# Kernel tuning notes

Measured on AMD Instinct MI355X. Metric: run time of the kernel, lower is better.

## Reference

```python
import jax, jax.numpy as jnp
import numpy as np

HEADS = 8

def _ln(x, g, b):
    m = jnp.mean(x, -1, keepdims=True)
    v = jnp.mean((x - m) ** 2, -1, keepdims=True)
    return (x - m) * jax.lax.rsqrt(v + 1e-5) * g + b

def _l2n(t):
    n = jnp.sqrt(jnp.sum(t * t, -1, keepdims=True))
    return t / jnp.maximum(n, 1e-12)

def _xca(x, ln_g, ln_b, w_qkv, temp, w_out, b_out):
    B, H, W, D = x.shape
    n = H * W
    xf = x.reshape(B, n, D)
    h = _ln(xf, ln_g, ln_b)
    qkv = h @ w_qkv  # [B, n, 3*inner]
    q, k, v = jnp.split(qkv, 3, axis=-1)
    def tohd(t):
        return t.reshape(B, n, HEADS, -1).transpose(0, 2, 3, 1)  # b h d n
    q, k, v = tohd(q), tohd(k), tohd(v)
    q, k = _l2n(q), _l2n(k)
    sim = jnp.einsum('bhdn,bhen->bhde', q, k) * jnp.exp(temp)[None, :, None, None]
    attn = jax.nn.softmax(sim, axis=-1)
    out = jnp.einsum('bhde,bhen->bhdn', attn, v)
    out = out.transpose(0, 3, 1, 2).reshape(B, n, -1)  # b n (h d)
    return (out @ w_out + b_out).reshape(B, H, W, D)

def _dwconv(x, w, b):
    # x: [B,C,H,W], w: [C,1,k,k] depthwise
    y = jax.lax.conv_general_dilated(x, w, (1, 1), 'SAME',
                                     feature_group_count=x.shape[1],
                                     dimension_numbers=('NCHW', 'OIHW', 'NCHW'))
    return y + b[None, :, None, None]

def _lpi(x, ln_g, ln_b, w1, b1, bn_g, bn_b, w2, b2):
    h = _ln(x, ln_g, ln_b).transpose(0, 3, 1, 2)  # b c h w
    h = _dwconv(h, w1, b1)
    # BatchNorm2d (training-mode batch stats, biased var, eps=1e-5)
    m = jnp.mean(h, (0, 2, 3), keepdims=True)
    v = jnp.mean((h - m) ** 2, (0, 2, 3), keepdims=True)
    h = (h - m) * jax.lax.rsqrt(v + 1e-5) * bn_g[None, :, None, None] + bn_b[None, :, None, None]
    h = jax.nn.gelu(h, approximate=False)
    h = _dwconv(h, w2, b2)
    return h.transpose(0, 2, 3, 1)

def _ff(x, g, b, w1, b1, w2, b2):
    h = _ln(x, g, b)
    h = jax.nn.gelu(h @ w1 + b1, approximate=False)
    return h @ w2 + b2

def setup_inputs() -> dict:
    key = jax.random.key(0)
    D, depth, Hh, dh, M = 384, 4, 8, 48, 1536
    inner = Hh * dh
    B, H, W = 16, 48, 48
    ks = jax.random.split(key, 8)
    x = jax.random.normal(ks[0], (B, H, W, D), jnp.float32)
    def nrm(k, shape, s=0.02):
        return jax.random.normal(k, shape, jnp.float32) * s
    return dict(
        x=x,
        ln1_g=jnp.ones((depth, D)), ln1_b=jnp.zeros((depth, D)),
        w_qkv=nrm(ks[1], (depth, D, 3 * inner)),
        temp=jnp.ones((depth, Hh)),
        w_out=nrm(ks[2], (depth, inner, D)), b_out=jnp.zeros((depth, D)),
        scale_attn=jnp.full((depth, D), 0.1, jnp.float32),
        lpi_ln_g=jnp.ones((depth, D)), lpi_ln_b=jnp.zeros((depth, D)),
        conv1_w=nrm(ks[3], (depth, D, 1, 3, 3), 0.1), conv1_b=jnp.zeros((depth, D)),
        bn_g=jnp.ones((depth, D)), bn_b=jnp.zeros((depth, D)),
        conv2_w=nrm(ks[4], (depth, D, 1, 3, 3), 0.1), conv2_b=jnp.zeros((depth, D)),
        scale_lpi=jnp.full((depth, D), 0.1, jnp.float32),
        ff_ln_g=jnp.ones((depth, D)), ff_ln_b=jnp.zeros((depth, D)),
        w1=nrm(ks[5], (depth, D, M)), b1=jnp.zeros((depth, M)),
        w2=nrm(ks[6], (depth, M, D)), b2=jnp.zeros((depth, D)),
        scale_ff=jnp.full((depth, D), 0.1, jnp.float32),
    )

def reference(x, ln1_g, ln1_b, w_qkv, temp, w_out, b_out, scale_attn,
              lpi_ln_g, lpi_ln_b, conv1_w, conv1_b, bn_g, bn_b, conv2_w, conv2_b, scale_lpi,
              ff_ln_g, ff_ln_b, w1, b1, w2, b2, scale_ff):
    depth = ln1_g.shape[0]
    for i in range(depth):
        x = _xca(x, ln1_g[i], ln1_b[i], w_qkv[i], temp[i], w_out[i], b_out[i]) * scale_attn[i] + x
        x = _lpi(x, lpi_ln_g[i], lpi_ln_b[i], conv1_w[i], conv1_b[i], bn_g[i], bn_b[i], conv2_w[i], conv2_b[i]) * scale_lpi[i] + x
        x = _ff(x, ff_ln_g[i], ff_ln_b[i], w1[i], b1[i], w2[i], b2[i]) * scale_ff[i] + x
    return x
```

## Files before the change

### kernel.cpp

```cpp
#include <hip/hip_runtime.h>
#include <math.h>

typedef unsigned short u16;
typedef unsigned int   u32;
typedef u16   u16x8 __attribute__((ext_vector_type(8)));
typedef u16   u16x4 __attribute__((ext_vector_type(4)));
typedef short s16x8 __attribute__((ext_vector_type(8)));
typedef float f32x4 __attribute__((ext_vector_type(4)));

#define DEVFN static __device__ __forceinline__
#define GLOBAL_AS __attribute__((address_space(1)))
#define LDS_AS    __attribute__((address_space(3)))

constexpr int Bb = 16, Hh = 48, Ww = 48, Dd = 384;
constexpr int Nn = Hh * Ww;
constexpr int NT = Bb * Nn;
constexpr int NH = 8, DHd = 48;
constexpr int INNER = NH * DHd;
constexpr int QC = 3 * INNER;
constexpr int MF = 1536;
constexpr int DEPTH = 4;
constexpr int NCH = 6;

DEVFN float bf2f(u16 u) { return __uint_as_float(((u32)u) << 16); }
DEVFN u16   f2bu(float f) { u32 x = __float_as_uint(f); return (u16)((x + 0x7FFFu + ((x >> 16) & 1u)) >> 16); }
DEVFN float geluf(float x) { return 0.5f * x * (1.0f + erff(x * 0.70710678118654752440f)); }

DEVFN void gload16(const u16* g, u16* lds_base) {
    __builtin_amdgcn_global_load_lds((const GLOBAL_AS void*)g, (LDS_AS void*)lds_base, 16, 0, 0);
}

__global__ void k_copy(const float* __restrict__ in, float* __restrict__ X) {
    size_t i0 = ((size_t)blockIdx.x * 256 + threadIdx.x) * 4;
    *(f32x4*)(X + i0) = *(const f32x4*)(in + i0);
}

__global__ __launch_bounds__(256) void k_trb(const float* __restrict__ in, u16* __restrict__ out,
                                             int K, int N) {
    __shared__ float tile[64][65];
    in  += (size_t)blockIdx.z * K * N;
    out += (size_t)blockIdx.z * K * N;
    int k0 = blockIdx.y * 64, n0 = blockIdx.x * 64;
    int t = threadIdx.x;
    int r = t >> 4, c = (t & 15) * 4;
#pragma unroll
    for (int j = 0; j < 4; j++) {
        f32x4 v = *(const f32x4*)&in[(size_t)(k0 + r + j * 16) * N + n0 + c];
        tile[r + j * 16][c] = v[0]; tile[r + j * 16][c + 1] = v[1];
        tile[r + j * 16][c + 2] = v[2]; tile[r + j * 16][c + 3] = v[3];
    }
    __syncthreads();
#pragma unroll
    for (int j = 0; j < 4; j++) {
        u16x4 o;
#pragma unroll
        for (int i = 0; i < 4; i++) o[i] = f2bu(tile[c + i][r + j * 16]);
        *(u16x4*)&out[(size_t)(n0 + r + j * 16) * K + k0 + c] = o;
    }
}

__global__ __launch_bounds__(256) void k_ln(const float* __restrict__ X,
                                            const float* __restrict__ g, const float* __restrict__ bta,
                                            u16* __restrict__ out) {
    int row = blockIdx.x * 4 + (threadIdx.x >> 6);
    int lane = threadIdx.x & 63;
    const float* xr = X + (size_t)row * Dd;
    float v[6]; float s = 0.f, s2 = 0.f;
#pragma unroll
    for (int j = 0; j < 6; j++) { v[j] = xr[lane + 64 * j]; s += v[j]; s2 += v[j] * v[j]; }
#pragma unroll
    for (int off = 32; off >= 1; off >>= 1) { s += __shfl_down(s, off); s2 += __shfl_down(s2, off); }
    s = __shfl(s, 0); s2 = __shfl(s2, 0);
    float m = s * (1.0f / Dd);
    float rstd = 1.0f / sqrtf(s2 * (1.0f / Dd) - m * m + 1e-5f);
    u16* orow = out + (size_t)row * Dd;
#pragma unroll
    for (int j = 0; j < 6; j++) {
        int c = lane + 64 * j;
        orow[c] = f2bu((v[j] - m) * rstd * g[c] + bta[c]);
    }
}

__global__ __launch_bounds__(256) void k_lnstat(const float* __restrict__ X, float* __restrict__ LNS) {
    int row = blockIdx.x * 4 + (threadIdx.x >> 6);
    int lane = threadIdx.x & 63;
    const float* xr = X + (size_t)row * Dd;
    float s = 0.f, s2 = 0.f;
#pragma unroll
    for (int j = 0; j < 6; j++) { float v = xr[lane + 64 * j]; s += v; s2 += v * v; }
#pragma unroll
    for (int off = 32; off >= 1; off >>= 1) { s += __shfl_down(s, off); s2 += __shfl_down(s2, off); }
    if (lane == 0) {
        float m = s * (1.0f / Dd);
        float rstd = 1.0f / sqrtf(s2 * (1.0f / Dd) - m * m + 1e-5f);
        LNS[row * 2] = m;
        LNS[row * 2 + 1] = rstd;
    }
}

template <int MODE>
__global__ __launch_bounds__(512, 4) void k_mgemm(const u16* __restrict__ A, const u16* __restrict__ BT,
                                                  int Kdim, int Ndim,
                                                  const float* __restrict__ bias, const float* __restrict__ scale,
                                                  float* __restrict__ Xres, u16* __restrict__ Out) {
    __shared__ __align__(16) u16 Ts[3][24 * 512];
    const int gridX = Ndim >> 7;
    const int nwg = gridX * (NT >> 8);
    const int cpx = nwg >> 3;
    const int id = blockIdx.x;
    const int id2 = (id & 7) * cpx + (id >> 3);
    const int n0 = (id2 % gridX) * 128;
    const int m0 = (id2 / gridX) * 256;
    const int t = threadIdx.x;
    const int w = t >> 6, l = t & 63;
    const int wm = w >> 1, wn = w & 1;
    const int lr = l >> 2;
    const int sc = ((l & 3) ^ (lr & 3)) * 8;
    const int fr = l & 15, rq = l >> 4;
    const int c0 = w * 3;

    auto stage = [&](int buf, int k0) {
#pragma unroll
        for (int j = 0; j < 3; j++) {
            const int c = c0 + j;
            const u16* src = (c < 16)
                ? A  + (size_t)(m0 + c * 16 + lr) * Kdim + k0 + sc
                : BT + (size_t)(n0 + (c - 16) * 16 + lr) * Kdim + k0 + sc;
            gload16(src, Ts[buf] + c * 512);
        }
    };

    const int nt = Kdim >> 5;
    stage(0, 0);
    stage(1, 32);

    f32x4 acc[4][4] = {};
    for (int kt = 0; kt < nt; ++kt) {
        if (kt + 1 < nt) {
            asm volatile("s_waitcnt vmcnt(3)" ::: "memory");
        } else {
            asm volatile("s_waitcnt vmcnt(0)" ::: "memory");
        }
        __builtin_amdgcn_s_barrier();
        __builtin_amdgcn_sched_barrier(0);
        if (kt + 2 < nt) stage((kt + 2) % 3, (kt + 2) * 32);
        const u16* ts = Ts[kt % 3];
        s16x8 af[4], bf[4];
#pragma unroll
        for (int f = 0; f < 4; f++) {
            const int row = wm * 64 + f * 16 + fr;
            af[f] = *(const s16x8*)&ts[row * 32 + ((rq ^ (fr & 3)) * 8)];
        }
#pragma unroll
        for (int g = 0; g < 4; g++) {
            const int row = wn * 64 + g * 16 + fr;
            bf[g] = *(const s16x8*)&ts[8192 + row * 32 + ((rq ^ (fr & 3)) * 8)];
        }
#pragma unroll
        for (int f = 0; f < 4; f++)
#pragma unroll
            for (int g = 0; g < 4; g++)
                acc[f][g] = __builtin_amdgcn_mfma_f32_16x16x32_bf16(af[f], bf[g], acc[f][g], 0, 0, 0);
    }
#pragma unroll
    for (int g = 0; g < 4; g++) {
        const int n = n0 + wn * 64 + g * 16 + fr;
        float bv = (MODE != 0) ? bias[n] : 0.f;
        float sv = (MODE == 2) ? scale[n] : 0.f;
#pragma unroll
        for (int f = 0; f < 4; f++) {
            const size_t i0 = (size_t)(m0 + wm * 64 + f * 16 + rq * 4);
#pragma unroll
            for (int r = 0; r < 4; r++) {
                float v = acc[f][g][r];
                if (MODE == 0) {
                    Out[(i0 + r) * Ndim + n] = f2bu(v);
                } else if (MODE == 1) {
                    Out[(i0 + r) * Ndim + n] = f2bu(geluf(v + bv));
                } else {
                    float* xr = Xres + (i0 + r) * Ndim + n;
                    *xr += sv * (v + bv);
                }
            }
        }
    }
}

__global__ __launch_bounds__(256) void k_nrm_part(const u16* __restrict__ QKV, float* __restrict__ part) {
    int b = blockIdx.x, s = blockIdx.y;
    int t = threadIdx.x;
    float a0 = 0, a1 = 0, a2 = 0;
    for (int r = s * 96; r < (s + 1) * 96; r++) {
        const u16* row = QKV + (size_t)(b * Nn + r) * QC;
        float v0 = bf2f(row[t]), v1 = bf2f(row[t + 256]), v2 = bf2f(row[t + 512]);
        a0 += v0 * v0; a1 += v1 * v1; a2 += v2 * v2;
    }
    float* o = part + (size_t)(b * 24 + s) * 768;
    o[t] = a0; o[t + 256] = a1; o[t + 512] = a2;
}

__global__ void k_nrm_fin(const float* __restrict__ part, float* __restrict__ INVN) {
    int idx = blockIdx.x * 256 + threadIdx.x;
    int b = idx / 768, c = idx - b * 768;
    float s = 0;
#pragma unroll
    for (int k = 0; k < 24; k++) s += part[(size_t)(b * 24 + k) * 768 + c];
    INVN[idx] = 1.0f / fmaxf(sqrtf(s), 1e-12f);
}

__global__ __launch_bounds__(256) void k_sim(const u16* __restrict__ QKV, float* __restrict__ SIMP) {
    const int bh = blockIdx.x;
    const int b = bh >> 3, h = bh & 7;
    const int chunk = blockIdx.y;
    __shared__ float qt[48][65];
    __shared__ float kt[48][65];
    const int t = threadIdx.x;
    const int w = t >> 6, l = t & 63;
    const int fr = l & 15, rq = l >> 4;
    const int ti0 = w, ti1 = w + 4;
    f32x4 acc0 = {}, acc1 = {}, acc2 = {};

    auto doTile = [&](int ti, f32x4& a) {
        const int d0 = (ti / 3) * 16, e0 = (ti % 3) * 16;
#pragma unroll
        for (int s = 0; s < 2; s++) {
            const float* qp = &qt[d0 + fr][s * 32 + rq * 8];
            const float* kp = &kt[e0 + fr][s * 32 + rq * 8];
            s16x8 af, bf;
#pragma unroll
            for (int j = 0; j < 8; j++) {
                af[j] = (short)(__float_as_uint(qp[j]) >> 16);
                bf[j] = (short)(__float_as_uint(kp[j]) >> 16);
            }
            a = __builtin_amdgcn_mfma_f32_16x16x32_bf16(af, bf, a, 0, 0, 0);
        }
    };

    for (int c0 = chunk * (Nn / NCH); c0 < (chunk + 1) * (Nn / NCH); c0 += 64) {
        __syncthreads();
        for (int e = t; e < 48 * 64; e += 256) {
            int r = e / 48, d = e - r * 48;
            const u16* p = QKV + (size_t)(b * Nn + c0 + r) * QC + h * DHd + d;
            qt[d][r] = bf2f(p[0]);
            kt[d][r] = bf2f(p[INNER]);
        }
        __syncthreads();
        doTile(ti0, acc0);
        doTile(ti1, acc1);
        if (w == 0) doTile(8, acc2);
    }

    float* so = SIMP + ((size_t)chunk * (Bb * NH) + bh) * (DHd * DHd);
    auto wr = [&](int ti, const f32x4& a) {
        const int d0 = (ti / 3) * 16, e0 = (ti % 3) * 16;
#pragma unroll
        for (int r = 0; r < 4; r++) so[(d0 + rq * 4 + r) * DHd + e0 + fr] = a[r];
    };
    wr(ti0, acc0);
    wr(ti1, acc1);
    if (w == 0) wr(8, acc2);
}

__global__ __launch_bounds__(256) void k_smax(const float* __restrict__ SIMP, float* __restrict__ SIM,
                                              const float* __restrict__ INVN, const float* __restrict__ temp) {
    int wid = blockIdx.x * 4 + (threadIdx.x >> 6);
    int lane = threadIdx.x & 63;
    int b = wid / (NH * DHd); int rem = wid - b * NH * DHd; int h = rem / DHd; int d = rem - h * DHd;
    int bh = b * NH + h;
    float et = expf(temp[h]);
    float invq = INVN[b * 768 + h * DHd + d];
    float myv = 0.f, mv = -3.0e38f;
    if (lane < DHd) {
        float s = 0.f;
#pragma unroll
        for (int c = 0; c < NCH; c++)
            s += SIMP[((size_t)c * (Bb * NH) + bh) * (DHd * DHd) + d * DHd + lane];
        myv = s * invq * INVN[b * 768 + 384 + h * DHd + lane] * et;
        mv = myv;
    }
#pragma unroll
    for (int off = 32; off >= 1; off >>= 1) mv = fmaxf(mv, __shfl_down(mv, off));
    mv = __shfl(mv, 0);
    float e = (lane < DHd) ? expf(myv - mv) : 0.f;
    float s = e;
#pragma unroll
    for (int off = 32; off >= 1; off >>= 1) s += __shfl_down(s, off);
    s = __shfl(s, 0);
    if (lane < DHd) SIM[(size_t)bh * (DHd * DHd) + d * DHd + lane] = e / s;
}

__global__ __launch_bounds__(256) void k_av(const u16* __restrict__ QKV, const float* __restrict__ SIM,
                                            u16* __restrict__ AOUT) {
    const int bh = blockIdx.x;
    const int b = bh >> 3, h = bh & 7;
    __shared__ __align__(16) float at[48][52];
    const int t = threadIdx.x;
    for (int e = t; e < 48 * 48; e += 256) at[e / 48][e % 48] = SIM[(size_t)bh * (DHd * DHd) + e];
    __syncthreads();
    const int r = blockIdx.y * 256 + t;
    const u16x8* vp = (const u16x8*)(QKV + (size_t)(b * Nn + r) * QC + 2 * INNER + h * DHd);
    f32x4 vv[12];
#pragma unroll
    for (int q8 = 0; q8 < 6; q8++) {
        u16x8 u = vp[q8];
#pragma unroll
        for (int j = 0; j < 8; j++) vv[q8 * 2 + (j >> 2)][j & 3] = bf2f(u[j]);
    }
    u16x8 ob[6];
#pragma unroll
    for (int d = 0; d < 48; d++) {
        f32x4 sv = {0.f, 0.f, 0.f, 0.f};
#pragma unroll
        for (int e4 = 0; e4 < 12; e4++) sv += *(const f32x4*)&at[d][e4 * 4] * vv[e4];
        ob[d >> 3][d & 7] = f2bu(sv[0] + sv[1] + sv[2] + sv[3]);
    }
    u16x8* orow = (u16x8*)(AOUT + (size_t)(b * Nn + r) * Dd + h * DHd);
#pragma unroll
    for (int q8 = 0; q8 < 6; q8++) orow[q8] = ob[q8];
}

__global__ __launch_bounds__(384) void k_lpi1(const float* __restrict__ X, const float* __restrict__ LNS,
                                              const float* __restrict__ g, const float* __restrict__ bta,
                                              const float* __restrict__ wgt, const float* __restrict__ cbias,
                                              u16* __restrict__ CF, float* __restrict__ BNP) {
    const int c = threadIdx.x;
    const int by = blockIdx.x;
    const int y = by % Hh, b = by / Hh;
    const int x0 = blockIdx.y * (Ww / 2);
    float w9[9];
#pragma unroll
    for (int j = 0; j < 9; j++) w9[j] = wgt[c * 9 + j];
    const float gc = g[c], bc = bta[c], cb = cbias[c];
    const size_t base = (size_t)b * Nn * Dd;
    const float* lns = LNS + (size_t)b * Nn * 2;

    auto load3 = [&](int xx, float* col) {
        if (xx < 0 || xx >= Ww) { col[0] = col[1] = col[2] = 0.f; return; }
#pragma unroll
        for (int dy = 0; dy < 3; dy++) {
            int yy = y + dy - 1;
            if (yy < 0 || yy >= Hh) { col[dy] = 0.f; }
            else {
                int tok = yy * Ww + xx;
                float m = lns[tok * 2], r = lns[tok * 2 + 1];
                col[dy] = (X[base + (size_t)tok * Dd + c] - m) * r * gc + bc;
            }
        }
    };

    float A[3], B[3], C[3], T[3];
    load3(x0 - 1, A); load3(x0, B); load3(x0 + 1, C);
    float s = 0.f, s2 = 0.f;
    u16* crow = CF + base + ((size_t)y * Ww + x0) * Dd + c;
    for (int x = x0; x < x0 + Ww / 2; x++) {
        load3(x + 2, T);
        float acc = cb;
#pragma unroll
        for (int dy = 0; dy < 3; dy++)
            acc += w9[dy * 3] * A[dy] + w9[dy * 3 + 1] * B[dy] + w9[dy * 3 + 2] * C[dy];
        crow[(size_t)(x - x0) * Dd] = f2bu(acc);
        s += acc; s2 += acc * acc;
#pragma unroll
        for (int dy = 0; dy < 3; dy++) { A[dy] = B[dy]; B[dy] = C[dy]; C[dy] = T[dy]; }
    }
    float* o = BNP + ((size_t)by * 2 + blockIdx.y) * 768;
    o[c] = s; o[384 + c] = s2;
}

__global__ __launch_bounds__(384) void k_bnred1(const float* __restrict__ BNP, float* __restrict__ BNQ) {
    int t = threadIdx.x, blk = blockIdx.x;
    float s = 0.f, s2 = 0.f;
    for (int i = blk * 24; i < blk * 24 + 24; i++) { s += BNP[(size_t)i * 768 + t]; s2 += BNP[(size_t)i * 768 + 384 + t]; }
    BNQ[(size_t)blk * 768 + t] = s; BNQ[(size_t)blk * 768 + 384 + t] = s2;
}

__global__ __launch_bounds__(384) void k_bnred2(const float* __restrict__ BNQ,
                                                const float* __restrict__ bng, const float* __restrict__ bnb,
                                                float* __restrict__ BNC) {
    int t = threadIdx.x;
    float s = 0.f, s2 = 0.f;
    for (int i = 0; i < 64; i++) { s += BNQ[(size_t)i * 768 + t]; s2 += BNQ[(size_t)i * 768 + 384 + t]; }
    float m = s / NT;
    float var = s2 / NT - m * m;
    float r = 1.0f / sqrtf(var + 1e-5f);
    BNC[t] = r * bng[t];
    BNC[384 + t] = bnb[t] - m * r * bng[t];
}

__global__ __launch_bounds__(384) void k_lpi2(const u16* __restrict__ CF, const float* __restrict__ BNC,
                                              const float* __restrict__ wgt, const float* __restrict__ cbias,
                                              const float* __restrict__ scale, float* __restrict__ X) {
    const int c = threadIdx.x;
    const int by = blockIdx.x;
    const int y = by % Hh, b = by / Hh;
    const int x0 = blockIdx.y * (Ww / 2);
    float w9[9];
#pragma unroll
    for (int j = 0; j < 9; j++) w9[j] = wgt[c * 9 + j];
    const float bnA = BNC[c], bnB = BNC[384 + c];
    const float cb = cbias[c], sc = scale[c];
    const size_t base = (size_t)b * Nn * Dd;

    auto load3 = [&](int xx, float* col) {
        if (xx < 0 || xx >= Ww) { col[0] = col[1] = col[2] = 0.f; return; }
#pragma unroll
        for (int dy = 0; dy < 3; dy++) {
            int yy = y + dy - 1;
            if (yy < 0 || yy >= Hh) { col[dy] = 0.f; }
            else {
                int tok = yy * Ww + xx;
                col[dy] = geluf(bf2f(CF[base + (size_t)tok * Dd + c]) * bnA + bnB);
            }
        }
    };

    float A[3], B[3], C[3], T[3];
    load3(x0 - 1, A); load3(x0, B); load3(x0 + 1, C);
    float* xrow = X + base + ((size_t)y * Ww + x0) * Dd + c;
    for (int x = x0; x < x0 + Ww / 2; x++) {
        load3(x + 2, T);
        float acc = cb;
#pragma unroll
        for (int dy = 0; dy < 3; dy++)
            acc += w9[dy * 3] * A[dy] + w9[dy * 3 + 1] * B[dy] + w9[dy * 3 + 2] * C[dy];
        xrow[(size_t)(x - x0) * Dd] += sc * acc;
#pragma unroll
        for (int dy = 0; dy < 3; dy++) { A[dy] = B[dy]; B[dy] = C[dy]; C[dy] = T[dy]; }
    }
}

extern "C" void kernel_launch(void* const* d_in, const int* in_sizes, int n_in,
                              void* d_out, int out_size, void* d_ws, size_t ws_size,
                              hipStream_t stream) {
    const float* x     = (const float*)d_in[0];
    const float* ln1_g = (const float*)d_in[1];
    const float* ln1_b = (const float*)d_in[2];
    const float* w_qkv = (const float*)d_in[3];
    const float* temp  = (const float*)d_in[4];
    const float* w_out = (const float*)d_in[5];
    const float* b_out = (const float*)d_in[6];
    const float* s_att = (const float*)d_in[7];
    const float* lpi_g = (const float*)d_in[8];
    const float* lpi_b = (const float*)d_in[9];
    const float* c1w   = (const float*)d_in[10];
    const float* c1b   = (const float*)d_in[11];
    const float* bng   = (const float*)d_in[12];
    const float* bnb   = (const float*)d_in[13];
    const float* c2w   = (const float*)d_in[14];
    const float* c2b   = (const float*)d_in[15];
    const float* s_lpi = (const float*)d_in[16];
    const float* ff_g  = (const float*)d_in[17];
    const float* ff_b  = (const float*)d_in[18];
    const float* w1    = (const float*)d_in[19];
    const float* b1    = (const float*)d_in[20];
    const float* w2    = (const float*)d_in[21];
    const float* b2    = (const float*)d_in[22];
    const float* s_ff  = (const float*)d_in[23];

    float* X = (float*)d_out;

    char* p = (char*)d_ws;
    auto carve = [&](size_t bytes) -> char* { char* r = p; p += (bytes + 255) / 256 * 256; return r; };
    u16*   BIG  = (u16*)  carve((size_t)NT * MF * 2);
    u16*   Hb   = (u16*)  carve((size_t)NT * Dd * 2);
    float* SIM  = (float*)carve((size_t)Bb * NH * DHd * DHd * 4);
    float* SIMP = (float*)carve((size_t)NCH * Bb * NH * DHd * DHd * 4);
    float* INVN = (float*)carve((size_t)Bb * 768 * 4);
    float* NPART= (float*)carve((size_t)Bb * 24 * 768 * 4);
    float* LNS  = (float*)carve((size_t)NT * 2 * 4);
    float* BNP  = (float*)carve((size_t)1536 * 768 * 4);
    float* BNQ  = (float*)carve((size_t)64 * 768 * 4);
    float* BNC  = (float*)carve((size_t)768 * 4);
    u16*   WQT  = (u16*)  carve((size_t)DEPTH * Dd * QC * 2);
    u16*   WOT  = (u16*)  carve((size_t)DEPTH * INNER * Dd * 2);
    u16*   W1T  = (u16*)  carve((size_t)DEPTH * Dd * MF * 2);
    u16*   W2T  = (u16*)  carve((size_t)DEPTH * MF * Dd * 2);
    u16*   AO   = BIG + (size_t)NT * QC;
    u16*   CF   = BIG;

    k_trb<<<dim3(QC / 64, Dd / 64, DEPTH), 256, 0, stream>>>(w_qkv, WQT, Dd, QC);
    k_trb<<<dim3(Dd / 64, INNER / 64, DEPTH), 256, 0, stream>>>(w_out, WOT, INNER, Dd);
    k_trb<<<dim3(MF / 64, Dd / 64, DEPTH), 256, 0, stream>>>(w1, W1T, Dd, MF);
    k_trb<<<dim3(Dd / 64, MF / 64, DEPTH), 256, 0, stream>>>(w2, W2T, MF, Dd);

    k_copy<<<NT * Dd / 1024, 256, 0, stream>>>(x, X);
    for (int L = 0; L < DEPTH; L++) {
        k_ln<<<NT / 4, 256, 0, stream>>>(X, ln1_g + L * Dd, ln1_b + L * Dd, Hb);
        k_mgemm<0><<<(QC / 128) * (NT / 256), 512, 0, stream>>>(Hb, WQT + (size_t)L * Dd * QC, Dd, QC,
                                                                nullptr, nullptr, nullptr, BIG);
        k_nrm_part<<<dim3(Bb, 24), 256, 0, stream>>>(BIG, NPART);
        k_nrm_fin<<<Bb * 768 / 256, 256, 0, stream>>>(NPART, INVN);
        k_sim<<<dim3(Bb * NH, NCH), 256, 0, stream>>>(BIG, SIMP);
        k_smax<<<Bb * NH * DHd / 4, 256, 0, stream>>>(SIMP, SIM, INVN, temp + L * NH);
        k_av<<<dim3(Bb * NH, Nn / 256), 256, 0, stream>>>(BIG, SIM, AO);
        k_mgemm<2><<<(Dd / 128) * (NT / 256), 512, 0, stream>>>(AO, WOT + (size_t)L * INNER * Dd, INNER, Dd,
                                                                b_out + L * Dd, s_att + L * Dd, X, nullptr);
        k_lnstat<<<NT / 4, 256, 0, stream>>>(X, LNS);
        k_lpi1<<<dim3(Bb * Hh, 2), 384, 0, stream>>>(X, LNS, lpi_g + L * Dd, lpi_b + L * Dd,
                                                     c1w + (size_t)L * Dd * 9, c1b + L * Dd, CF, BNP);
        k_bnred1<<<64, 384, 0, stream>>>(BNP, BNQ);
        k_bnred2<<<1, 384, 0, stream>>>(BNQ, bng + L * Dd, bnb + L * Dd, BNC);
        k_lpi2<<<dim3(Bb * Hh, 2), 384, 0, stream>>>(CF, BNC, c2w + (size_t)L * Dd * 9, c2b + L * Dd,
                                                     s_lpi + L * Dd, X);
        k_ln<<<NT / 4, 256, 0, stream>>>(X, ff_g + L * Dd, ff_b + L * Dd, Hb);
        k_mgemm<1><<<(MF / 128) * (NT / 256), 512, 0, stream>>>(Hb, W1T + (size_t)L * Dd * MF, Dd, MF,
                                                                b1 + L * MF, nullptr, nullptr, BIG);
        k_mgemm<2><<<(Dd / 128) * (NT / 256), 512, 0, stream>>>(BIG, W2T + (size_t)L * MF * Dd, MF, Dd,
                                                                b2 + L * Dd, s_ff + L * Dd, X, nullptr);
    }
}
```

Measured before the change: 2.123 ms.

## Fuse Q/K norm sums into QKV GEMM epilogue and FF LayerNorm into LPI conv

The QKV GEMM gains a mode that accumulates per-column sums of squares for the q and k columns in its epilogue. Each workgroup writes a partial to a small buffer, which replaces the separate pass that re-read the whole QKV output. The second LPI depthwise-conv kernel now stages its updated residual rows in LDS, computes the FF LayerNorm, and writes the bf16 normalized activations directly, removing a standalone LN kernel and its re-read of X. Norms are now taken from fp32 accumulators instead of rounded bf16 values, a small numerical difference. The larger LDS footprint in k_lpi2 and the extra epilogue work in the GEMM may reduce occupancy.

Measured after the change: 2.138 ms. Within noise of the previous version (+0.7%).

```diff
diff --git a/kernel.cpp b/kernel.cpp
--- a/kernel.cpp
+++ b/kernel.cpp
@@ -102,8 +102,10 @@
 __global__ __launch_bounds__(512, 4) void k_mgemm(const u16* __restrict__ A, const u16* __restrict__ BT,
                                                   int Kdim, int Ndim,
                                                   const float* __restrict__ bias, const float* __restrict__ scale,
-                                                  float* __restrict__ Xres, u16* __restrict__ Out) {
+                                                  float* __restrict__ Xres, u16* __restrict__ Out,
+                                                  float* __restrict__ QP) {
     __shared__ __align__(16) u16 Ts[3][24 * 512];
+    __shared__ float QS[4][128];
     const int gridX = Ndim >> 7;
     const int nwg = gridX * (NT >> 8);
     const int cpx = nwg >> 3;
@@ -162,10 +164,12 @@
             for (int g = 0; g < 4; g++)
                 acc[f][g] = __builtin_amdgcn_mfma_f32_16x16x32_bf16(af[f], bf[g], acc[f][g], 0, 0, 0);
     }
+
+    float sq[4] = {0.f, 0.f, 0.f, 0.f};
 #pragma unroll
     for (int g = 0; g < 4; g++) {
         const int n = n0 + wn * 64 + g * 16 + fr;
-        float bv = (MODE != 0) ? bias[n] : 0.f;
+        float bv = (MODE == 1 || MODE == 2) ? bias[n] : 0.f;
         float sv = (MODE == 2) ? scale[n] : 0.f;
 #pragma unroll
         for (int f = 0; f < 4; f++) {
@@ -173,8 +177,9 @@
 #pragma unroll
             for (int r = 0; r < 4; r++) {
                 float v = acc[f][g][r];
-                if (MODE == 0) {
+                if (MODE == 0 || MODE == 3) {
                     Out[(i0 + r) * Ndim + n] = f2bu(v);
+                    if (MODE == 3) sq[g] += v * v;
                 } else if (MODE == 1) {
                     Out[(i0 + r) * Ndim + n] = f2bu(geluf(v + bv));
                 } else {
@@ -184,27 +189,30 @@
             }
         }
     }
-}
-
-__global__ __launch_bounds__(256) void k_nrm_part(const u16* __restrict__ QKV, float* __restrict__ part) {
-    int b = blockIdx.x, s = blockIdx.y;
-    int t = threadIdx.x;
-    float a0 = 0, a1 = 0, a2 = 0;
-    for (int r = s * 96; r < (s + 1) * 96; r++) {
-        const u16* row = QKV + (size_t)(b * Nn + r) * QC;
-        float v0 = bf2f(row[t]), v1 = bf2f(row[t + 256]), v2 = bf2f(row[t + 512]);
-        a0 += v0 * v0; a1 += v1 * v1; a2 += v2 * v2;
-    }
-    float* o = part + (size_t)(b * 24 + s) * 768;
-    o[t] = a0; o[t + 256] = a1; o[t + 512] = a2;
-}
-
-__global__ void k_nrm_fin(const float* __restrict__ part, float* __restrict__ INVN) {
+
+    if (MODE == 3 && n0 < 768) {
+#pragma unroll
+        for (int g = 0; g < 4; g++) {
+            float s2 = sq[g];
+            s2 += __shfl_down(s2, 32);
+            s2 += __shfl_down(s2, 16);
+            if (rq == 0) QS[wm][wn * 64 + g * 16 + fr] = s2;
+        }
+        __syncthreads();
+        if (t < 128) {
+            float s = QS[0][t] + QS[1][t] + QS[2][t] + QS[3][t];
+            const int b_img = m0 / Nn, mset = (m0 % Nn) >> 8;
+            QP[((size_t)(b_img * 9 + mset)) * 768 + n0 + t] = s;
+        }
+    }
+}
+
+__global__ void k_nrm_fin(const float* __restrict__ QP, float* __restrict__ INVN) {
     int idx = blockIdx.x * 256 + threadIdx.x;
     int b = idx / 768, c = idx - b * 768;
     float s = 0;
 #pragma unroll
-    for (int k = 0; k < 24; k++) s += part[(size_t)(b * 24 + k) * 768 + c];
+    for (int ms = 0; ms < 9; ms++) s += QP[((size_t)(b * 9 + ms)) * 768 + c];
     INVN[idx] = 1.0f / fmaxf(sqrtf(s), 1e-12f);
 }
 
@@ -389,7 +397,11 @@
 
 __global__ __launch_bounds__(384) void k_lpi2(const u16* __restrict__ CF, const float* __restrict__ BNC,
                                               const float* __restrict__ wgt, const float* __restrict__ cbias,
-                                              const float* __restrict__ scale, float* __restrict__ X) {
+                                              const float* __restrict__ scale, float* __restrict__ X,
+                                              const float* __restrict__ ffg, const float* __restrict__ ffb,
+                                              u16* __restrict__ Hb) {
+    __shared__ float XS[24][388];
+    __shared__ float MS[24][2];
     const int c = threadIdx.x;
     const int by = blockIdx.x;
     const int y = by % Hh, b = by / Hh;
@@ -423,9 +435,37 @@
 #pragma unroll
         for (int dy = 0; dy < 3; dy++)
             acc += w9[dy * 3] * A[dy] + w9[dy * 3 + 1] * B[dy] + w9[dy * 3 + 2] * C[dy];
-        xrow[(size_t)(x - x0) * Dd] += sc * acc;
+        float xnew = xrow[(size_t)(x - x0) * Dd] + sc * acc;
+        xrow[(size_t)(x - x0) * Dd] = xnew;
+        XS[x - x0][c] = xnew;
 #pragma unroll
         for (int dy = 0; dy < 3; dy++) { A[dy] = B[dy]; B[dy] = C[dy]; C[dy] = T[dy]; }
+    }
+    __syncthreads();
+
+    const int wv = c >> 6, lane = c & 63;
+#pragma unroll
+    for (int k = 0; k < 4; k++) {
+        const int tt = wv * 4 + k;
+        float s = 0.f, s2 = 0.f;
+#pragma unroll
+        for (int j = 0; j < 6; j++) { float v = XS[tt][lane + 64 * j]; s += v; s2 += v * v; }
+#pragma unroll
+        for (int off = 32; off >= 1; off >>= 1) { s += __shfl_down(s, off); s2 += __shfl_down(s2, off); }
+        if (lane == 0) {
+            float m = s * (1.0f / Dd);
+            MS[tt][0] = m;
+            MS[tt][1] = 1.0f / sqrtf(s2 * (1.0f / Dd) - m * m + 1e-5f);
+        }
+    }
+    __syncthreads();
+
+    const float gc = ffg[c], bc2 = ffb[c];
+    u16* hrow = Hb + base + ((size_t)y * Ww + x0) * Dd + c;
+#pragma unroll 4
+    for (int x = 0; x < 24; x++) {
+        float h = (XS[x][c] - MS[x][0]) * MS[x][1] * gc + bc2;
+        hrow[(size_t)x * Dd] = f2bu(h);
     }
 }
 
@@ -466,7 +506,7 @@
     float* SIM  = (float*)carve((size_t)Bb * NH * DHd * DHd * 4);
     float* SIMP = (float*)carve((size_t)NCH * Bb * NH * DHd * DHd * 4);
     float* INVN = (float*)carve((size_t)Bb * 768 * 4);
-    float* NPART= (float*)carve((size_t)Bb * 24 * 768 * 4);
+    float* QP   = (float*)carve((size_t)Bb * 9 * 768 * 4);
     float* LNS  = (float*)carve((size_t)NT * 2 * 4);
     float* BNP  = (float*)carve((size_t)1536 * 768 * 4);
     float* BNQ  = (float*)carve((size_t)64 * 768 * 4);
@@ -486,26 +526,24 @@
     k_copy<<<NT * Dd / 1024, 256, 0, stream>>>(x, X);
     for (int L = 0; L < DEPTH; L++) {
         k_ln<<<NT / 4, 256, 0, stream>>>(X, ln1_g + L * Dd, ln1_b + L * Dd, Hb);
-        k_mgemm<0><<<(QC / 128) * (NT / 256), 512, 0, stream>>>(Hb, WQT + (size_t)L * Dd * QC, Dd, QC,
-                                                                nullptr, nullptr, nullptr, BIG);
-        k_nrm_part<<<dim3(Bb, 24), 256, 0, stream>>>(BIG, NPART);
-        k_nrm_fin<<<Bb * 768 / 256, 256, 0, stream>>>(NPART, INVN);
+        k_mgemm<3><<<(QC / 128) * (NT / 256), 512, 0, stream>>>(Hb, WQT + (size_t)L * Dd * QC, Dd, QC,
+                                                                nullptr, nullptr, nullptr, BIG, QP);
+        k_nrm_fin<<<Bb * 768 / 256, 256, 0, stream>>>(QP, INVN);
         k_sim<<<dim3(Bb * NH, NCH), 256, 0, stream>>>(BIG, SIMP);
         k_smax<<<Bb * NH * DHd / 4, 256, 0, stream>>>(SIMP, SIM, INVN, temp + L * NH);
         k_av<<<dim3(Bb * NH, Nn / 256), 256, 0, stream>>>(BIG, SIM, AO);
         k_mgemm<2><<<(Dd / 128) * (NT / 256), 512, 0, stream>>>(AO, WOT + (size_t)L * INNER * Dd, INNER, Dd,
-                                                                b_out + L * Dd, s_att + L * Dd, X, nullptr);
+                                                                b_out + L * Dd, s_att + L * Dd, X, nullptr, nullptr);
         k_lnstat<<<NT / 4, 256, 0, stream>>>(X, LNS);
         k_lpi1<<<dim3(Bb * Hh, 2), 384, 0, stream>>>(X, LNS, lpi_g + L * Dd, lpi_b + L * Dd,
                                                      c1w + (size_t)L * Dd * 9, c1b + L * Dd, CF, BNP);
         k_bnred1<<<64, 384, 0, stream>>>(BNP, BNQ);
         k_bnred2<<<1, 384, 0, stream>>>(BNQ, bng + L * Dd, bnb + L * Dd, BNC);
         k_lpi2<<<dim3(Bb * Hh, 2), 384, 0, stream>>>(CF, BNC, c2w + (size_t)L * Dd * 9, c2b + L * Dd,
-                                                     s_lpi + L * Dd, X);
-        k_ln<<<NT / 4, 256, 0, stream>>>(X, ff_g + L * Dd, ff_b + L * Dd, Hb);
+                                                     s_lpi + L * Dd, X, ff_g + L * Dd, ff_b + L * Dd, Hb);
         k_mgemm<1><<<(MF / 128) * (NT / 256), 512, 0, stream>>>(Hb, W1T + (size_t)L * Dd * MF, Dd, MF,
-                                                                b1 + L * MF, nullptr, nullptr, BIG);
+                                                                b1 + L * MF, nullptr, nullptr, BIG, nullptr);
         k_mgemm<2><<<(Dd / 128) * (NT / 256), 512, 0, stream>>>(BIG, W2T + (size_t)L * MF * Dd, MF, Dd,
-                                                                b2 + L * Dd, s_ff + L * Dd, X, nullptr);
-    }
-}
+                                                                b2 + L * Dd, s_ff + L * Dd, X, nullptr, nullptr);
+    }
+}
```
